# Performance work log

Hardware: AMD Instinct MI355X
Metric: run time of the kernel (lower is better)

The kernel has to match this reference:

```python
import jax, jax.numpy as jnp
from jax import lax
import numpy as np

GROUPS = 32

def setup_inputs() -> dict:
    key = jax.random.key(0)
    ks = jax.random.split(key, 12)
    B, C, H, O, N = 4, 256, 256, 256, 4096
    s = 0.02  # small init scale to keep logits in a stable range
    x  = jax.random.normal(ks[0], (B, C, N), dtype=jnp.float32)
    Wk = jax.random.normal(ks[1], (H, C), dtype=jnp.float32) * s
    bk = jax.random.normal(ks[2], (H,), dtype=jnp.float32) * s
    Wq = jax.random.normal(ks[3], (H, C), dtype=jnp.float32) * s
    bq = jax.random.normal(ks[4], (H,), dtype=jnp.float32) * s
    W1 = jax.random.normal(ks[5], (H, C), dtype=jnp.float32) * s
    b1 = jax.random.normal(ks[6], (H,), dtype=jnp.float32) * s
    # grouped conv1d kernel: (out_ch, in_ch // groups, kw) in 'OIH' layout
    W2 = jax.random.normal(ks[7], (H, H // GROUPS, 3), dtype=jnp.float32) * s
    b2 = jax.random.normal(ks[8], (H,), dtype=jnp.float32) * s
    W3 = jax.random.normal(ks[9], (O, H), dtype=jnp.float32) * s
    b3 = jax.random.normal(ks[10], (O,), dtype=jnp.float32) * s
    return {"x": x, "Wk": Wk, "bk": bk, "Wq": Wq, "bq": bq,
            "W1": W1, "b1": b1, "W2": W2, "b2": b2, "W3": W3, "b3": b3}


def reference(x, Wk, bk, Wq, bq, W1, b1, W2, b2, W3, b3):
    # k: 1x1 conv then permute(0,2,1) -> [B, N, H]
    k = jnp.einsum('hc,bcn->bnh', Wk, x) + bk
    # q: 1x1 conv -> [B, H, N]
    q = jnp.einsum('hc,bcn->bhn', Wq, x) + bq[None, :, None]
    # sim = softmax(k @ q, dim=-2): softmax over the FIRST N axis (rows)
    sim = jax.nn.softmax(jnp.einsum('bnh,bhm->bnm', k, q), axis=-2)  # [B, N, N]
    # v path: 1x1 conv -> grouped 3-tap conv (pad=1) -> ReLU -> 1x1 conv
    v1 = jnp.einsum('hc,bcn->bhn', W1, x) + b1[None, :, None]
    v2 = lax.conv_general_dilated(
        v1, W2, window_strides=(1,), padding='SAME',
        feature_group_count=GROUPS,
        dimension_numbers=('NCH', 'OIH', 'NCH')) + b2[None, :, None]
    v2 = jax.nn.relu(v2)
    v = jnp.einsum('oh,bhn->bon', W3, v2) + b3[None, :, None]  # [B, O, N]
    # out = v @ sim -> [B, O, N]
    return jnp.einsum('bon,bnm->bom', v, sim)
```

## Files before the change

kernel.cpp:

```cpp
#include <hip/hip_runtime.h>


#define B_ 4
#define C_ 256
#define H_ 256
#define O_ 256
#define N_ 4096
#define NSPLIT 4
#define SPAN (N_ / NSPLIT)
#define ITERS (SPAN / 32)

typedef short short8 __attribute__((ext_vector_type(8)));
typedef float floatx4 __attribute__((ext_vector_type(4)));
typedef float floatx16 __attribute__((ext_vector_type(16)));
typedef unsigned uint2v __attribute__((ext_vector_type(2)));

__device__ __forceinline__ unsigned short f2bf(float f) {
  unsigned u = __float_as_uint(f);
  u = (u + 0x7fffu + ((u >> 16) & 1u)) >> 16;
  return (unsigned short)u;
}
__device__ __forceinline__ float bf2f(unsigned short u) {
  return __uint_as_float(((unsigned)u) << 16);
}
__device__ __forceinline__ floatx4 mfma16(short8 a, short8 b, floatx4 c) {
  return __builtin_amdgcn_mfma_f32_16x16x32_bf16(a, b, c, 0, 0, 0);
}
__device__ __forceinline__ floatx16 mfma32(short8 a, short8 b, floatx16 c) {
  return __builtin_amdgcn_mfma_f32_32x32x16_bf16(a, b, c, 0, 0, 0);
}
__device__ __forceinline__ unsigned pack2bf(float a, float b) {
  return __builtin_amdgcn_perm(__float_as_uint(b) + 0x8000u,
                               __float_as_uint(a) + 0x8000u, 0x07060302u);
}

__global__ __launch_bounds__(256) void prep_transpose_kernel(
    const float* __restrict__ x, unsigned short* __restrict__ xt,
    const float* __restrict__ Wk, const float* __restrict__ Wq,
    const float* __restrict__ W1, const float* __restrict__ W3,
    unsigned short* __restrict__ wk, unsigned short* __restrict__ wq,
    unsigned short* __restrict__ w1, unsigned short* __restrict__ w3) {
  __shared__ unsigned short tile[64][66];
  const int gid = blockIdx.x;
  const int t = threadIdx.x;
  if (gid >= 1024) {
    const int i = (gid - 1024) * 256 + t;
    wk[i] = f2bf(Wk[i]);
    wq[i] = f2bf(Wq[i]);
    w1[i] = f2bf(W1[i]);
    w3[i] = f2bf(W3[i]);
    return;
  }
  const int b  = gid >> 8;
  const int ct = (gid >> 6) & 3;
  const int nt = gid & 63;
  const int c0 = ct * 64, n0 = nt * 64;
  const float* xb = x + ((size_t)b * C_ + c0) * N_ + n0;
#pragma unroll
  for (int rr = 0; rr < 4; ++rr) {
    const int c = (t >> 4) + rr * 16;
    const floatx4 v = *reinterpret_cast<const floatx4*>(
        xb + (size_t)c * N_ + (t & 15) * 4);
#pragma unroll
    for (int i = 0; i < 4; ++i) tile[c][(t & 15) * 4 + i] = f2bf(v[i]);
  }
  __syncthreads();
  unsigned short* xo = xt + ((size_t)b * N_ + n0) * C_ + c0;
#pragma unroll
  for (int rr = 0; rr < 2; ++rr) {
    const int nr = (t >> 3) + rr * 32;
    short8 pk;
#pragma unroll
    for (int i = 0; i < 8; ++i) pk[i] = (short)tile[(t & 7) * 8 + i][nr];
    *reinterpret_cast<short8*>(xo + (size_t)nr * C_ + (t & 7) * 8) = pk;
  }
}

__global__ __launch_bounds__(256) void gemm1_kernel(
    const unsigned short* __restrict__ xt,
    const unsigned short* __restrict__ wk, const unsigned short* __restrict__ wq,
    const unsigned short* __restrict__ w1,
    const float* __restrict__ bk, const float* __restrict__ bq,
    const float* __restrict__ b1,
    unsigned short* __restrict__ ko, unsigned short* __restrict__ qo,
    unsigned short* __restrict__ v1o) {
  const int lane = threadIdx.x & 63;
  const int wid  = blockIdx.x * 4 + (threadIdx.x >> 6);
  const int b  = wid >> 9;
  const int r  = wid & 511;
  const int hh = r >> 8;
  const int nt = r & 255;
  const int n0 = nt * 16;
  const int m  = lane & 15;
  const int q  = lane >> 4;

  const unsigned short* xrow = xt + ((size_t)(b * N_) + n0 + m) * C_;
  const unsigned short* Ws[3] = {wk, wq, w1};

  floatx4 acc[3][8];
  const floatx4 z = {0.f, 0.f, 0.f, 0.f};
#pragma unroll
  for (int o = 0; o < 3; ++o)
#pragma unroll
    for (int tt = 0; tt < 8; ++tt) acc[o][tt] = z;

  for (int cs = 0; cs < 8; ++cs) {
    const int cb = cs * 32 + q * 8;
    short8 af = *reinterpret_cast<const short8*>(xrow + cb);
#pragma unroll
    for (int o = 0; o < 3; ++o) {
#pragma unroll
      for (int tt = 0; tt < 8; ++tt) {
        const int h0 = (hh * 8 + tt) * 16;
        short8 bf = *reinterpret_cast<const short8*>(Ws[o] + (h0 + m) * C_ + cb);
        acc[o][tt] = mfma16(af, bf, acc[o][tt]);
      }
    }
  }

  const int msw = m ^ ((q & 1) << 3);
#pragma unroll
  for (int tt = 0; tt < 8; ++tt) {
    const int ks16 = hh * 8 + tt;
    const float bias = bk[ks16 * 16 + m];
#pragma unroll
    for (int r2 = 0; r2 < 4; ++r2) {
      const int n = n0 + q * 4 + r2;
      ko[((size_t)(b * 128 + (n >> 5))) * 8192 + ks16 * 512 + (n & 31) * 16 + msw] =
          f2bf(acc[0][tt][r2] + bias);
    }
  }
  const float* biases[2] = {bq, b1};
  unsigned short* outs[2] = {qo, v1o};
#pragma unroll
  for (int o = 0; o < 2; ++o) {
#pragma unroll
    for (int tt = 0; tt < 8; ++tt) {
      const int h0 = (hh * 8 + tt) * 16;
      const float bias = biases[o][h0 + m];
#pragma unroll
      for (int r2 = 0; r2 < 4; ++r2) {
        const int n = n0 + q * 4 + r2;
        outs[o][(b * N_ + n) * H_ + h0 + m] = f2bf(acc[o + 1][tt][r2] + bias);
      }
    }
  }
}

__global__ __launch_bounds__(256) void convgemm2_kernel(
    const unsigned short* __restrict__ v1, const float* __restrict__ W2,
    const float* __restrict__ b2, const unsigned short* __restrict__ w3,
    const float* __restrict__ b3, unsigned short* __restrict__ vo) {
  __shared__ unsigned short v2L[32][264];

  const int h   = threadIdx.x;
  const int blk = blockIdx.x;
  const int b   = blk >> 7;
  const int nc  = blk & 127;
  const int n0  = nc * 32;
  const int g8  = h & ~7;

  {
    float w[24];
#pragma unroll
    for (int i = 0; i < 24; ++i) w[i] = W2[h * 24 + i];
    const float bias = b2[h];
    const unsigned short* vb = v1 + (size_t)b * (N_ * H_) + g8;

    float fp[8], fc[8], fn[8];
    if (n0 == 0) {
#pragma unroll
      for (int i = 0; i < 8; ++i) fp[i] = 0.f;
    } else {
      short8 u = *reinterpret_cast<const short8*>(vb + (size_t)(n0 - 1) * H_);
#pragma unroll
      for (int i = 0; i < 8; ++i) fp[i] = bf2f((unsigned short)u[i]);
    }
    {
      short8 u = *reinterpret_cast<const short8*>(vb + (size_t)n0 * H_);
#pragma unroll
      for (int i = 0; i < 8; ++i) fc[i] = bf2f((unsigned short)u[i]);
    }
#pragma unroll 1
    for (int ns = 0; ns < 32; ++ns) {
      const int n = n0 + ns;
      if (n + 1 < N_) {
        short8 u = *reinterpret_cast<const short8*>(vb + (size_t)(n + 1) * H_);
#pragma unroll
        for (int i = 0; i < 8; ++i) fn[i] = bf2f((unsigned short)u[i]);
      } else {
#pragma unroll
        for (int i = 0; i < 8; ++i) fn[i] = 0.f;
      }
      float a = bias;
#pragma unroll
      for (int i = 0; i < 8; ++i)
        a += w[i * 3] * fp[i] + w[i * 3 + 1] * fc[i] + w[i * 3 + 2] * fn[i];
      v2L[ns][h] = f2bf(fmaxf(a, 0.f));
#pragma unroll
      for (int i = 0; i < 8; ++i) { fp[i] = fc[i]; fc[i] = fn[i]; }
    }
  }
  __syncthreads();

  const int ln = threadIdx.x & 63;
  const int wv = threadIdx.x >> 6;
  const int m  = ln & 31;
  const int hl = ln >> 5;

  floatx16 acc2[2];
#pragma unroll
  for (int ot = 0; ot < 2; ++ot)
#pragma unroll
    for (int r = 0; r < 16; ++r) acc2[ot][r] = 0.f;

#pragma unroll
  for (int ks = 0; ks < 16; ++ks) {
    short8 bfr = *reinterpret_cast<const short8*>(&v2L[m][ks * 16 + hl * 8]);
#pragma unroll
    for (int ot = 0; ot < 2; ++ot) {
      const int o0 = wv * 64 + ot * 32;
      short8 afr = *reinterpret_cast<const short8*>(
          w3 + (o0 + m) * H_ + ks * 16 + hl * 8);
      acc2[ot] = mfma32(afr, bfr, acc2[ot]);
    }
  }

  const int kn  = (m >> 4) & 1;
  const int nsw = (m & 15) ^ (hl << 3);
  unsigned short* vkn = vo + ((size_t)(b * 128 + nc) * 2 + kn) * 4096;
#pragma unroll
  for (int ot = 0; ot < 2; ++ot)
#pragma unroll
    for (int r = 0; r < 16; ++r) {
      const int o = wv * 64 + ot * 32 + (r & 3) + 8 * (r >> 2) + 4 * hl;
      vkn[o * 16 + nsw] = f2bf(acc2[ot][r] + b3[o]);
    }
}

__global__ __launch_bounds__(256, 2) void attn_kernel(
    const unsigned short* __restrict__ kbf, const unsigned short* __restrict__ qbf,
    const unsigned short* __restrict__ vbf,
    unsigned short* __restrict__ pacc, float* __restrict__ pml) {
  __shared__ __attribute__((aligned(16))) char smem[2][32768];

  const int ln  = threadIdx.x & 63;
  const int wv  = threadIdx.x >> 6;
  const int gid = blockIdx.x;
  const int b   = gid & 3;
  const int s   = (gid >> 2) & 3;
  const int mt128 = gid >> 4;
  const int mt32  = mt128 * 4 + wv;
  const int m0  = mt32 * 32;
  const int m   = ln & 31;
  const int hl  = ln >> 5;
  const int lane_base = m * 32 + (hl ^ ((m >> 2) & 1)) * 16;

  const unsigned short* qrow = qbf + ((size_t)b * N_ + m0 + m) * H_ + hl * 8;
  short8 qf[16];
#pragma unroll
  for (int ks = 0; ks < 16; ++ks)
    qf[ks] = *reinterpret_cast<const short8*>(qrow + ks * 16);

  floatx16 acc[8];
#pragma unroll
  for (int t = 0; t < 8; ++t)
#pragma unroll
    for (int r = 0; r < 16; ++r) acc[t][r] = 0.f;
  float Lp = 0.f;

  auto stage = [&](int bfi, int nc) {
    const size_t row = (size_t)(b * 128 + s * 32 + nc);
    const char* kg = (const char*)(kbf + row * 8192);
    const char* vg = (const char*)(vbf + row * 8192);
    char* lk = &smem[bfi][0];
    char* lv = &smem[bfi][16384];
#pragma unroll
    for (int j = 0; j < 4; ++j) {
      const int ofs = j * 4096 + wv * 1024 + ln * 16;
      __builtin_amdgcn_global_load_lds(
          (const __attribute__((address_space(1))) void*)(kg + ofs),
          (__attribute__((address_space(3))) void*)(lk + ofs), 16, 0, 0);
      __builtin_amdgcn_global_load_lds(
          (const __attribute__((address_space(1))) void*)(vg + ofs),
          (__attribute__((address_space(3))) void*)(lv + ofs), 16, 0, 0);
    }
  };

  stage(0, 0);
  int bufi = 0;

#pragma unroll 1
  for (int nc = 0; nc < ITERS; ++nc) {
    __syncthreads();
    if (nc + 1 < ITERS) stage(bufi ^ 1, nc + 1);

    const char* sk = &smem[bufi][0];
    const char* sv = &smem[bufi][16384];

    floatx16 sacc;
#pragma unroll
    for (int r = 0; r < 16; ++r) sacc[r] = 0.f;
#pragma unroll
    for (int ks = 0; ks < 16; ++ks) {
      short8 kf = *reinterpret_cast<const short8*>(sk + lane_base + ks * 1024);
      sacc = mfma32(kf, qf[ks], sacc);
    }

    short8 pf0, pf1;
#if __has_builtin(__builtin_amdgcn_permlane32_swap)
    unsigned d[8];
#pragma unroll
    for (int i = 0; i < 8; ++i) {
      const float a = __expf(sacc[2 * i]);
      const float bb = __expf(sacc[2 * i + 1]);
      Lp += a + bb;
      d[i] = pack2bf(a, bb);
    }
#pragma unroll
    for (int g = 0; g < 2; ++g) {
      uint2v r0 = __builtin_amdgcn_permlane32_swap(d[4 * g + 0], d[4 * g + 2],
                                                   false, false);
      uint2v r1 = __builtin_amdgcn_permlane32_swap(d[4 * g + 1], d[4 * g + 3],
                                                   false, false);
      d[4 * g + 0] = r0.x; d[4 * g + 2] = r0.y;
      d[4 * g + 1] = r1.x; d[4 * g + 3] = r1.y;
    }
    union { unsigned u[4]; short8 s8; } c0, c1;
    c0.u[0] = d[0]; c0.u[1] = d[1]; c0.u[2] = d[2]; c0.u[3] = d[3];
    c1.u[0] = d[4]; c1.u[1] = d[5]; c1.u[2] = d[6]; c1.u[3] = d[7];
    pf0 = c0.s8;
    pf1 = c1.s8;
#else
    float pv[16];
#pragma unroll
    for (int r = 0; r < 16; ++r) { pv[r] = __expf(sacc[r]); Lp += pv[r]; }
    unsigned wpk[8];
#pragma unroll
    for (int r4 = 0; r4 < 4; ++r4) {
      wpk[r4]     = pack2bf(pv[r4], pv[r4 + 4]);
      wpk[r4 + 4] = pack2bf(pv[r4 + 8], pv[r4 + 12]);
    }
    const int hlsh = hl * 16;
#pragma unroll
    for (int j = 0; j < 8; ++j) {
      const int srcLane = m + ((j >> 2) << 5);
      const int u0 = __shfl((int)wpk[j & 3],       srcLane);
      const int u1 = __shfl((int)wpk[(j & 3) + 4], srcLane);
      pf0[j] = (short)((unsigned)u0 >> hlsh);
      pf1[j] = (short)((unsigned)u1 >> hlsh);
    }
#endif

#pragma unroll
    for (int ot = 0; ot < 8; ++ot) {
      short8 vf0 = *reinterpret_cast<const short8*>(sv + lane_base + ot * 1024);
      short8 vf1 = *reinterpret_cast<const short8*>(
          sv + lane_base + 8192 + ot * 1024);
      acc[ot] = mfma32(vf0, pf0, acc[ot]);
      acc[ot] = mfma32(vf1, pf1, acc[ot]);
    }
    bufi ^= 1;
  }

  float Lv = Lp + __shfl_xor(Lp, 32);
  const float invL = 1.f / Lv;

  const int pwid = (b * 128 + mt32) * NSPLIT + s;
  unsigned short* pa = pacc + (size_t)pwid * (O_ * 32);
#pragma unroll
  for (int ot = 0; ot < 8; ++ot)
#pragma unroll
    for (int r = 0; r < 16; ++r) {
      const int o = ot * 32 + (r & 3) + 8 * (r >> 2) + 4 * hl;
      pa[o * 32 + m] = f2bf(acc[ot][r] * invL);
    }
  if (hl == 0) pml[pwid * 32 + m] = Lv;
}

__global__ __launch_bounds__(256) void combine_kernel(
    const unsigned short* __restrict__ pacc, const float* __restrict__ pml,
    float* __restrict__ out) {
  const int blk = blockIdx.x;
  const int b   = blk >> 7;
  const int mw  = blk & 127;
  const int o   = threadIdx.x;
  const int base = (b * 128 + mw) * NSPLIT;

  __shared__ float w[NSPLIT][32];
  if (threadIdx.x < 32) {
    const int c = threadIdx.x;
    float L[NSPLIT], sum = 0.f;
#pragma unroll
    for (int sp = 0; sp < NSPLIT; ++sp) {
      L[sp] = pml[(base + sp) * 32 + c];
      sum += L[sp];
    }
    const float inv = 1.f / sum;
#pragma unroll
    for (int sp = 0; sp < NSPLIT; ++sp) w[sp][c] = L[sp] * inv;
  }
  __syncthreads();

  float res[32];
#pragma unroll
  for (int c = 0; c < 32; ++c) res[c] = 0.f;
#pragma unroll
  for (int sp = 0; sp < NSPLIT; ++sp) {
    const unsigned short* pa =
        pacc + (size_t)(base + sp) * (O_ * 32) + o * 32;
#pragma unroll
    for (int c8 = 0; c8 < 4; ++c8) {
      short8 u = *reinterpret_cast<const short8*>(pa + c8 * 8);
#pragma unroll
      for (int i = 0; i < 8; ++i)
        res[c8 * 8 + i] =
            fmaf(w[sp][c8 * 8 + i], bf2f((unsigned short)u[i]), res[c8 * 8 + i]);
    }
  }
  float* ob = out + ((size_t)(b * O_ + o)) * N_ + mw * 32;
#pragma unroll
  for (int c4 = 0; c4 < 8; ++c4) {
    floatx4 v4 = {res[c4 * 4], res[c4 * 4 + 1], res[c4 * 4 + 2], res[c4 * 4 + 3]};
    *reinterpret_cast<floatx4*>(ob + c4 * 4) = v4;
  }
}

extern "C" void kernel_launch(void* const* d_in, const int* in_sizes, int n_in,
                              void* d_out, int out_size, void* d_ws, size_t ws_size,
                              hipStream_t stream) {
  const float* x  = (const float*)d_in[0];
  const float* Wk = (const float*)d_in[1];
  const float* bk = (const float*)d_in[2];
  const float* Wq = (const float*)d_in[3];
  const float* bq = (const float*)d_in[4];
  const float* W1 = (const float*)d_in[5];
  const float* b1 = (const float*)d_in[6];
  const float* W2 = (const float*)d_in[7];
  const float* b2 = (const float*)d_in[8];
  const float* W3 = (const float*)d_in[9];
  const float* b3 = (const float*)d_in[10];
  float* out = (float*)d_out;

  char* ws = (char*)d_ws;
  const size_t SZ = (size_t)B_ * N_ * H_ * sizeof(unsigned short);
  unsigned short* wkbf = (unsigned short*)(ws);
  unsigned short* wqbf = (unsigned short*)(ws + 131072);
  unsigned short* w1bf = (unsigned short*)(ws + 262144);
  unsigned short* w3bf = (unsigned short*)(ws + 393216);
  char* base = ws + 524288;
  unsigned short* kbf  = (unsigned short*)(base);
  unsigned short* qbf  = (unsigned short*)(base + SZ);
  unsigned short* vbf  = (unsigned short*)(base + 2 * SZ);
  unsigned short* xtbf = (unsigned short*)(base + 3 * SZ);
  unsigned short* v1bf = (unsigned short*)(base + 4 * SZ);
  unsigned short* pacc = (unsigned short*)(base + 3 * SZ);
  float*          pml  = (float*)(base + 7 * SZ);

  prep_transpose_kernel<<<1280, 256, 0, stream>>>(
      x, xtbf, Wk, Wq, W1, W3, wkbf, wqbf, w1bf, w3bf);
  gemm1_kernel<<<512, 256, 0, stream>>>(xtbf, wkbf, wqbf, w1bf, bk, bq, b1,
                                        kbf, qbf, v1bf);
  convgemm2_kernel<<<512, 256, 0, stream>>>(v1bf, W2, b2, w3bf, b3, vbf);
  attn_kernel<<<512, 256, 0, stream>>>(kbf, qbf, vbf, pacc, pml);
  combine_kernel<<<512, 256, 0, stream>>>(pacc, pml, out);
}
```

Before: 248.1 us.

## Fuse x transpose and weight bf16 conversion into projection and conv GEMM kernels

```diff
diff --git a/kernel.cpp b/kernel.cpp
--- a/kernel.cpp
+++ b/kernel.cpp
@@ -33,115 +33,108 @@
   return __builtin_amdgcn_perm(__float_as_uint(b) + 0x8000u,
                                __float_as_uint(a) + 0x8000u, 0x07060302u);
 }
-
-__global__ __launch_bounds__(256) void prep_transpose_kernel(
-    const float* __restrict__ x, unsigned short* __restrict__ xt,
+__device__ __forceinline__ short8 cvt8(const float* __restrict__ p) {
+  const floatx4 a = *reinterpret_cast<const floatx4*>(p);
+  const floatx4 b = *reinterpret_cast<const floatx4*>(p + 4);
+  union { unsigned u[4]; short8 s8; } r;
+  r.u[0] = pack2bf(a[0], a[1]);
+  r.u[1] = pack2bf(a[2], a[3]);
+  r.u[2] = pack2bf(b[0], b[1]);
+  r.u[3] = pack2bf(b[2], b[3]);
+  return r.s8;
+}
+
+__global__ __launch_bounds__(512) void gemm1_kernel(
+    const float* __restrict__ x,
     const float* __restrict__ Wk, const float* __restrict__ Wq,
-    const float* __restrict__ W1, const float* __restrict__ W3,
-    unsigned short* __restrict__ wk, unsigned short* __restrict__ wq,
-    unsigned short* __restrict__ w1, unsigned short* __restrict__ w3) {
-  __shared__ unsigned short tile[64][66];
-  const int gid = blockIdx.x;
-  const int t = threadIdx.x;
-  if (gid >= 1024) {
-    const int i = (gid - 1024) * 256 + t;
-    wk[i] = f2bf(Wk[i]);
-    wq[i] = f2bf(Wq[i]);
-    w1[i] = f2bf(W1[i]);
-    w3[i] = f2bf(W3[i]);
-    return;
-  }
-  const int b  = gid >> 8;
-  const int ct = (gid >> 6) & 3;
-  const int nt = gid & 63;
-  const int c0 = ct * 64, n0 = nt * 64;
-  const float* xb = x + ((size_t)b * C_ + c0) * N_ + n0;
-#pragma unroll
-  for (int rr = 0; rr < 4; ++rr) {
-    const int c = (t >> 4) + rr * 16;
-    const floatx4 v = *reinterpret_cast<const floatx4*>(
-        xb + (size_t)c * N_ + (t & 15) * 4);
-#pragma unroll
-    for (int i = 0; i < 4; ++i) tile[c][(t & 15) * 4 + i] = f2bf(v[i]);
-  }
-  __syncthreads();
-  unsigned short* xo = xt + ((size_t)b * N_ + n0) * C_ + c0;
-#pragma unroll
-  for (int rr = 0; rr < 2; ++rr) {
-    const int nr = (t >> 3) + rr * 32;
-    short8 pk;
-#pragma unroll
-    for (int i = 0; i < 8; ++i) pk[i] = (short)tile[(t & 7) * 8 + i][nr];
-    *reinterpret_cast<short8*>(xo + (size_t)nr * C_ + (t & 7) * 8) = pk;
-  }
-}
-
-__global__ __launch_bounds__(256) void gemm1_kernel(
-    const unsigned short* __restrict__ xt,
-    const unsigned short* __restrict__ wk, const unsigned short* __restrict__ wq,
-    const unsigned short* __restrict__ w1,
+    const float* __restrict__ W1,
     const float* __restrict__ bk, const float* __restrict__ bq,
     const float* __restrict__ b1,
     unsigned short* __restrict__ ko, unsigned short* __restrict__ qo,
     unsigned short* __restrict__ v1o) {
-  const int lane = threadIdx.x & 63;
-  const int wid  = blockIdx.x * 4 + (threadIdx.x >> 6);
-  const int b  = wid >> 9;
-  const int r  = wid & 511;
-  const int hh = r >> 8;
-  const int nt = r & 255;
-  const int n0 = nt * 16;
-  const int m  = lane & 15;
-  const int q  = lane >> 4;
-
-  const unsigned short* xrow = xt + ((size_t)(b * N_) + n0 + m) * C_;
-  const unsigned short* Ws[3] = {wk, wq, w1};
-
-  floatx4 acc[3][8];
-  const floatx4 z = {0.f, 0.f, 0.f, 0.f};
-#pragma unroll
-  for (int o = 0; o < 3; ++o)
-#pragma unroll
-    for (int tt = 0; tt < 8; ++tt) acc[o][tt] = z;
-
+  __shared__ unsigned short xT[64 * 264];
+
+  const int t   = threadIdx.x;
+  const int gid = blockIdx.x;
+  const int b   = gid >> 6;
+  const int n0  = (gid & 63) * 64;
+
+  {
+    const int nl = t & 63;
+    const int cg = t >> 6;
+    const int xsw = (nl >> 3) & 3;
+    const float* xb = x + (size_t)b * (C_ * N_) + n0 + nl;
+#pragma unroll 8
+    for (int cc = 0; cc < 32; ++cc) {
+      const int c = cc * 8 + cg;
+      xT[nl * 264 + (cc ^ xsw) * 8 + cg] = f2bf(xb[(size_t)c * N_]);
+    }
+  }
+  __syncthreads();
+
+  const int ln  = t & 63;
+  const int wv  = t >> 6;
+  const int ntw = wv & 3;
+  const int hhw = wv >> 2;
+  const int m   = ln & 15;
+  const int q   = ln >> 4;
+  const int row = ntw * 16 + m;
+  const int rsw = (row >> 3) & 3;
+
+  short8 af[8];
+#pragma unroll
   for (int cs = 0; cs < 8; ++cs) {
-    const int cb = cs * 32 + q * 8;
-    short8 af = *reinterpret_cast<const short8*>(xrow + cb);
-#pragma unroll
-    for (int o = 0; o < 3; ++o) {
+    const int gran = (cs * 4 + q) ^ rsw;
+    af[cs] = *reinterpret_cast<const short8*>(&xT[row * 264 + gran * 8]);
+  }
+
+  const float* Ws[3] = {Wk, Wq, W1};
+  const float* Bs[3] = {bk, bq, b1};
+  const int msw = m ^ ((q & 1) << 3);
+
+#pragma unroll
+  for (int o = 0; o < 3; ++o) {
+    floatx4 acc[8];
+    const floatx4 z = {0.f, 0.f, 0.f, 0.f};
+#pragma unroll
+    for (int tt = 0; tt < 8; ++tt) acc[tt] = z;
+
+    const float* W = Ws[o];
+#pragma unroll
+    for (int cs = 0; cs < 8; ++cs) {
+      const int cb = cs * 32 + q * 8;
 #pragma unroll
       for (int tt = 0; tt < 8; ++tt) {
-        const int h0 = (hh * 8 + tt) * 16;
-        short8 bf = *reinterpret_cast<const short8*>(Ws[o] + (h0 + m) * C_ + cb);
-        acc[o][tt] = mfma16(af, bf, acc[o][tt]);
+        const int h0 = (hhw * 8 + tt) * 16;
+        short8 bf = cvt8(W + (size_t)(h0 + m) * C_ + cb);
+        acc[tt] = mfma16(af[cs], bf, acc[tt]);
       }
     }
-  }
-
-  const int msw = m ^ ((q & 1) << 3);
-#pragma unroll
-  for (int tt = 0; tt < 8; ++tt) {
-    const int ks16 = hh * 8 + tt;
-    const float bias = bk[ks16 * 16 + m];
-#pragma unroll
-    for (int r2 = 0; r2 < 4; ++r2) {
-      const int n = n0 + q * 4 + r2;
-      ko[((size_t)(b * 128 + (n >> 5))) * 8192 + ks16 * 512 + (n & 31) * 16 + msw] =
-          f2bf(acc[0][tt][r2] + bias);
-    }
-  }
-  const float* biases[2] = {bq, b1};
-  unsigned short* outs[2] = {qo, v1o};
-#pragma unroll
-  for (int o = 0; o < 2; ++o) {
-#pragma unroll
-    for (int tt = 0; tt < 8; ++tt) {
-      const int h0 = (hh * 8 + tt) * 16;
-      const float bias = biases[o][h0 + m];
-#pragma unroll
-      for (int r2 = 0; r2 < 4; ++r2) {
-        const int n = n0 + q * 4 + r2;
-        outs[o][(b * N_ + n) * H_ + h0 + m] = f2bf(acc[o + 1][tt][r2] + bias);
+
+    if (o == 0) {
+#pragma unroll
+      for (int tt = 0; tt < 8; ++tt) {
+        const int ks16 = hhw * 8 + tt;
+        const float bias = bk[ks16 * 16 + m];
+#pragma unroll
+        for (int r2 = 0; r2 < 4; ++r2) {
+          const int n = n0 + ntw * 16 + q * 4 + r2;
+          ko[((size_t)(b * 128 + (n >> 5))) * 8192 + ks16 * 512 +
+             (n & 31) * 16 + msw] = f2bf(acc[tt][r2] + bias);
+        }
+      }
+    } else {
+      unsigned short* op = (o == 1) ? qo : v1o;
+      const float* bp = Bs[o];
+#pragma unroll
+      for (int tt = 0; tt < 8; ++tt) {
+        const int h0 = (hhw * 8 + tt) * 16;
+        const float bias = bp[h0 + m];
+#pragma unroll
+        for (int r2 = 0; r2 < 4; ++r2) {
+          const int n = n0 + ntw * 16 + q * 4 + r2;
+          op[(size_t)(b * N_ + n) * H_ + h0 + m] = f2bf(acc[tt][r2] + bias);
+        }
       }
     }
   }
@@ -149,7 +142,7 @@
 
 __global__ __launch_bounds__(256) void convgemm2_kernel(
     const unsigned short* __restrict__ v1, const float* __restrict__ W2,
-    const float* __restrict__ b2, const unsigned short* __restrict__ w3,
+    const float* __restrict__ b2, const float* __restrict__ w3,
     const float* __restrict__ b3, unsigned short* __restrict__ vo) {
   __shared__ unsigned short v2L[32][264];
 
@@ -181,7 +174,7 @@
 #pragma unroll
       for (int i = 0; i < 8; ++i) fc[i] = bf2f((unsigned short)u[i]);
     }
-#pragma unroll 1
+#pragma unroll 4
     for (int ns = 0; ns < 32; ++ns) {
       const int n = n0 + ns;
       if (n + 1 < N_) {
@@ -220,8 +213,7 @@
 #pragma unroll
     for (int ot = 0; ot < 2; ++ot) {
       const int o0 = wv * 64 + ot * 32;
-      short8 afr = *reinterpret_cast<const short8*>(
-          w3 + (o0 + m) * H_ + ks * 16 + hl * 8);
+      short8 afr = cvt8(w3 + (size_t)(o0 + m) * H_ + ks * 16 + hl * 8);
       acc2[ot] = mfma32(afr, bfr, acc2[ot]);
     }
   }
@@ -442,26 +434,18 @@
   const float* b3 = (const float*)d_in[10];
   float* out = (float*)d_out;
 
-  char* ws = (char*)d_ws;
+  char* base = (char*)d_ws;
   const size_t SZ = (size_t)B_ * N_ * H_ * sizeof(unsigned short);
-  unsigned short* wkbf = (unsigned short*)(ws);
-  unsigned short* wqbf = (unsigned short*)(ws + 131072);
-  unsigned short* w1bf = (unsigned short*)(ws + 262144);
-  unsigned short* w3bf = (unsigned short*)(ws + 393216);
-  char* base = ws + 524288;
   unsigned short* kbf  = (unsigned short*)(base);
   unsigned short* qbf  = (unsigned short*)(base + SZ);
   unsigned short* vbf  = (unsigned short*)(base + 2 * SZ);
-  unsigned short* xtbf = (unsigned short*)(base + 3 * SZ);
-  unsigned short* v1bf = (unsigned short*)(base + 4 * SZ);
+  unsigned short* v1bf = (unsigned short*)(base + 3 * SZ);
   unsigned short* pacc = (unsigned short*)(base + 3 * SZ);
   float*          pml  = (float*)(base + 7 * SZ);
 
-  prep_transpose_kernel<<<1280, 256, 0, stream>>>(
-      x, xtbf, Wk, Wq, W1, W3, wkbf, wqbf, w1bf, w3bf);
-  gemm1_kernel<<<512, 256, 0, stream>>>(xtbf, wkbf, wqbf, w1bf, bk, bq, b1,
+  gemm1_kernel<<<256, 512, 0, stream>>>(x, Wk, Wq, W1, bk, bq, b1,
                                         kbf, qbf, v1bf);
-  convgemm2_kernel<<<512, 256, 0, stream>>>(v1bf, W2, b2, w3bf, b3, vbf);
+  convgemm2_kernel<<<512, 256, 0, stream>>>(v1bf, W2, b2, W3, b3, vbf);
   attn_kernel<<<512, 256, 0, stream>>>(kbf, qbf, vbf, pacc, pml);
   combine_kernel<<<512, 256, 0, stream>>>(pacc, pml, out);
 }
```

Measured after the change: 286.4 us. 1.15x slower.
